# Performance work log

Measured on AMD Instinct MI355X. Metric: run time of the kernel, lower is better.

Reference implementation:

```python
import jax, jax.numpy as jnp
import numpy as np

N = 8192      # nodes
D_IN = 128    # input features
D_H = 48      # GAT hidden (hardcoded in module)
D_OUT = 32    # control output dim
NEG_INF = -9e15  # matches torch code's -9000000000000000.0


def setup_inputs() -> dict:
    key = jax.random.key(0)
    ks = jax.random.split(key, 12)
    s = 0.05
    return {
        "x": jax.random.normal(ks[0], (N, D_IN), jnp.float32),
        "adj": jax.random.randint(ks[1], (N, N), 0, 2, jnp.int32),
        "W_gat": jax.random.normal(ks[2], (D_H, D_IN), jnp.float32) * s,
        "a": jax.random.normal(ks[3], (1, D_H), jnp.float32) * s,
        "gamma": jnp.ones((D_H,), jnp.float32),
        "beta": jnp.zeros((D_H,), jnp.float32),
        "W1": jax.random.normal(ks[4], (256, D_H), jnp.float32) * s,
        "b1": jnp.zeros((256,), jnp.float32),
        "W2": jax.random.normal(ks[5], (128, 256), jnp.float32) * s,
        "b2": jnp.zeros((128,), jnp.float32),
        "W3": jax.random.normal(ks[6], (D_OUT, 128), jnp.float32) * s,
        "b3": jnp.zeros((D_OUT,), jnp.float32),
    }


def reference(x, adj, W_gat, a, gamma, beta, W1, b1, W2, b2, W3, b3):
    # --- LightweightGATLayer ---
    Wh = x @ W_gat.T                      # [N, D_H]
    s = Wh @ a.T                          # [N, 1] additive attention scores
    e = s + s.T                           # [N, N]
    e = jnp.where(e > 0, e, 0.2 * e)      # LeakyReLU(0.2)
    e = jnp.where(adj > 0, e, NEG_INF)    # mask non-edges
    attn = jax.nn.softmax(e, axis=1)      # row softmax; dropout is identity in eval
    h_prime = attn @ Wh                   # [N, D_H]
    # LayerNorm over last dim, eps=1e-5
    mu = jnp.mean(h_prime, axis=-1, keepdims=True)
    var = jnp.var(h_prime, axis=-1, keepdims=True)
    h = (h_prime - mu) * jax.lax.rsqrt(var + 1e-5) * gamma + beta
    # --- BiACT MLP head: 48 -> 256 -> 128 -> D_OUT ---
    h = jax.nn.relu(h @ W1.T + b1)
    h = jax.nn.relu(h @ W2.T + b2)
    return h @ W3.T + b3                  # [N, D_OUT]
```

## Files before the change

kernel.cpp:

```cpp
#include <hip/hip_runtime.h>

#define N 8192
#define DIN 128
#define DH 48
#define MT 128
#define KC 64
#define NSPLIT 16
#define JSPAN (N / NSPLIT)
#define NCHUNK (JSPAN / KC)
#define ACC_STRIDE 64
#define HSTR 49
#define RB 32

typedef _Float16 half8 __attribute__((ext_vector_type(8)));
typedef float f32x4 __attribute__((ext_vector_type(4)));

__global__ __launch_bounds__(256) void k_wh(const float* __restrict__ x,
                                            const float* __restrict__ Wg,
                                            float* __restrict__ Wh) {
    __shared__ float wT[DIN * DH];
    int t = threadIdx.x;
    for (int e = t; e < DIN * DH; e += 256) {
        int c = e / DIN, k = e % DIN;
        wT[k * DH + c] = Wg[e];
    }
    __syncthreads();
    int o = blockIdx.x * 256 + t;
    int r = o / DH, c = o % DH;
    const float4* xr = (const float4*)(x + (size_t)r * DIN);
    float acc = 0.f;
    #pragma unroll 8
    for (int k4 = 0; k4 < DIN / 4; ++k4) {
        float4 xv = xr[k4];
        int kb = k4 * 4;
        acc += xv.x * wT[(kb + 0) * DH + c];
        acc += xv.y * wT[(kb + 1) * DH + c];
        acc += xv.z * wT[(kb + 2) * DH + c];
        acc += xv.w * wT[(kb + 3) * DH + c];
    }
    Wh[o] = acc;
}

__global__ __launch_bounds__(256) void k_s(const float* __restrict__ Wh,
                                           const float* __restrict__ a,
                                           float* __restrict__ s) {
    int r = blockIdx.x * 256 + threadIdx.x;
    const float4* wr = (const float4*)(Wh + (size_t)r * DH);
    const float4* av = (const float4*)a;
    float acc = 0.f;
    #pragma unroll
    for (int k4 = 0; k4 < DH / 4; ++k4) {
        float4 w = wr[k4]; float4 aa = av[k4];
        acc += w.x * aa.x + w.y * aa.y + w.z * aa.z + w.w * aa.w;
    }
    s[r] = acc;
}

__global__ __launch_bounds__(256) void k_tr(const float* __restrict__ Wh,
                                            _Float16* __restrict__ WhT) {
    __shared__ _Float16 tile[DH][72];
    int t = threadIdx.x;
    int r0 = blockIdx.x * 64;
    for (int e = t; e < 64 * DH; e += 256) {
        int r = e / DH, c = e % DH;
        tile[c][r] = (_Float16)Wh[(size_t)(r0 + r) * DH + c];
    }
    __syncthreads();
    for (int u = t; u < DH * 8; u += 256) {
        int c = u >> 3, g = u & 7;
        *(half8*)&WhT[(size_t)c * N + r0 + g * 8] = *(const half8*)&tile[c][g * 8];
    }
}

__device__ inline half8 mk_p(float si, float4 sa, float4 sb, int4 m0, int4 m1) {
    float e0 = si + sa.x, e1 = si + sa.y, e2 = si + sa.z, e3 = si + sa.w;
    float e4 = si + sb.x, e5 = si + sb.y, e6 = si + sb.z, e7 = si + sb.w;
    e0 = fmaxf(e0, 0.2f * e0); e1 = fmaxf(e1, 0.2f * e1);
    e2 = fmaxf(e2, 0.2f * e2); e3 = fmaxf(e3, 0.2f * e3);
    e4 = fmaxf(e4, 0.2f * e4); e5 = fmaxf(e5, 0.2f * e5);
    e6 = fmaxf(e6, 0.2f * e6); e7 = fmaxf(e7, 0.2f * e7);
    half8 r;
    r[0] = (_Float16)(m0.x ? __expf(e0) : 0.f);
    r[1] = (_Float16)(m0.y ? __expf(e1) : 0.f);
    r[2] = (_Float16)(m0.z ? __expf(e2) : 0.f);
    r[3] = (_Float16)(m0.w ? __expf(e3) : 0.f);
    r[4] = (_Float16)(m1.x ? __expf(e4) : 0.f);
    r[5] = (_Float16)(m1.y ? __expf(e5) : 0.f);
    r[6] = (_Float16)(m1.z ? __expf(e6) : 0.f);
    r[7] = (_Float16)(m1.w ? __expf(e7) : 0.f);
    return r;
}

__global__ __launch_bounds__(256, 4) void k_gat(const int* __restrict__ adj,
                                                const _Float16* __restrict__ WhT,
                                                const float* __restrict__ s,
                                                float* __restrict__ accWs) {
    int t = threadIdx.x;
    int tile = blockIdx.x & 63;
    int split = blockIdx.x >> 6;
    int i0 = tile * MT;
    int jbase = split * JSPAN;

    int lane = t & 63, w = t >> 6;
    int ln16 = lane & 15, kq = lane >> 4;

    half8 bc;
    {
        _Float16 v = (ln16 == 0) ? (_Float16)1.0f : (_Float16)0.0f;
        #pragma unroll
        for (int i = 0; i < 8; ++i) bc[i] = v;
    }

    f32x4 acc[2][4];
    #pragma unroll
    for (int m = 0; m < 2; ++m)
        #pragma unroll
        for (int n = 0; n < 4; ++n) acc[m][n] = (f32x4){0.f, 0.f, 0.f, 0.f};

    const int row0 = i0 + w * 32 + ln16;
    const int row1 = row0 + 16;
    const float si0 = s[row0];
    const float si1 = s[row1];
    const int* ar0 = adj + (size_t)row0 * N;
    const int* ar1 = adj + (size_t)row1 * N;

    for (int chunk = 0; chunk < NCHUNK; ++chunk) {
        const int j0 = jbase + chunk * KC;
        const int jk0 = j0 + kq * 8;
        const int jk1 = jk0 + 32;

        int4 m00a = *(const int4*)(ar0 + jk0);
        int4 m00b = *(const int4*)(ar0 + jk0 + 4);
        int4 m01a = *(const int4*)(ar0 + jk1);
        int4 m01b = *(const int4*)(ar0 + jk1 + 4);
        int4 m10a = *(const int4*)(ar1 + jk0);
        int4 m10b = *(const int4*)(ar1 + jk0 + 4);
        int4 m11a = *(const int4*)(ar1 + jk1);
        int4 m11b = *(const int4*)(ar1 + jk1 + 4);
        float4 s0a = *(const float4*)(s + jk0);
        float4 s0b = *(const float4*)(s + jk0 + 4);
        float4 s1a = *(const float4*)(s + jk1);
        float4 s1b = *(const float4*)(s + jk1 + 4);
        half8 bf00 = *(const half8*)&WhT[(size_t)(0  + ln16) * N + jk0];
        half8 bf01 = *(const half8*)&WhT[(size_t)(16 + ln16) * N + jk0];
        half8 bf02 = *(const half8*)&WhT[(size_t)(32 + ln16) * N + jk0];
        half8 bf10 = *(const half8*)&WhT[(size_t)(0  + ln16) * N + jk1];
        half8 bf11 = *(const half8*)&WhT[(size_t)(16 + ln16) * N + jk1];
        half8 bf12 = *(const half8*)&WhT[(size_t)(32 + ln16) * N + jk1];

        half8 a00 = mk_p(si0, s0a, s0b, m00a, m00b);
        half8 a01 = mk_p(si0, s1a, s1b, m01a, m01b);
        half8 a10 = mk_p(si1, s0a, s0b, m10a, m10b);
        half8 a11 = mk_p(si1, s1a, s1b, m11a, m11b);

        acc[0][0] = __builtin_amdgcn_mfma_f32_16x16x32_f16(a00, bf00, acc[0][0], 0, 0, 0);
        acc[0][1] = __builtin_amdgcn_mfma_f32_16x16x32_f16(a00, bf01, acc[0][1], 0, 0, 0);
        acc[0][2] = __builtin_amdgcn_mfma_f32_16x16x32_f16(a00, bf02, acc[0][2], 0, 0, 0);
        acc[0][3] = __builtin_amdgcn_mfma_f32_16x16x32_f16(a00, bc,   acc[0][3], 0, 0, 0);
        acc[1][0] = __builtin_amdgcn_mfma_f32_16x16x32_f16(a10, bf00, acc[1][0], 0, 0, 0);
        acc[1][1] = __builtin_amdgcn_mfma_f32_16x16x32_f16(a10, bf01, acc[1][1], 0, 0, 0);
        acc[1][2] = __builtin_amdgcn_mfma_f32_16x16x32_f16(a10, bf02, acc[1][2], 0, 0, 0);
        acc[1][3] = __builtin_amdgcn_mfma_f32_16x16x32_f16(a10, bc,   acc[1][3], 0, 0, 0);
        acc[0][0] = __builtin_amdgcn_mfma_f32_16x16x32_f16(a01, bf10, acc[0][0], 0, 0, 0);
        acc[0][1] = __builtin_amdgcn_mfma_f32_16x16x32_f16(a01, bf11, acc[0][1], 0, 0, 0);
        acc[0][2] = __builtin_amdgcn_mfma_f32_16x16x32_f16(a01, bf12, acc[0][2], 0, 0, 0);
        acc[0][3] = __builtin_amdgcn_mfma_f32_16x16x32_f16(a01, bc,   acc[0][3], 0, 0, 0);
        acc[1][0] = __builtin_amdgcn_mfma_f32_16x16x32_f16(a11, bf10, acc[1][0], 0, 0, 0);
        acc[1][1] = __builtin_amdgcn_mfma_f32_16x16x32_f16(a11, bf11, acc[1][1], 0, 0, 0);
        acc[1][2] = __builtin_amdgcn_mfma_f32_16x16x32_f16(a11, bf12, acc[1][2], 0, 0, 0);
        acc[1][3] = __builtin_amdgcn_mfma_f32_16x16x32_f16(a11, bc,   acc[1][3], 0, 0, 0);
    }

    #pragma unroll
    for (int mtl = 0; mtl < 2; ++mtl) {
        size_t rbase = (size_t)split * N + i0 + w * 32 + mtl * 16 + kq * 4;
        #pragma unroll
        for (int nt = 0; nt < 4; ++nt) {
            int col = nt * 16 + ln16;
            if (nt == 3 && ln16 != 0) continue;
            #pragma unroll
            for (int reg = 0; reg < 4; ++reg)
                accWs[(rbase + reg) * ACC_STRIDE + col] = acc[mtl][nt][reg];
        }
    }
}

__global__ __launch_bounds__(256) void k_mlp(const float* __restrict__ accWs,
                                             const float* __restrict__ gamma,
                                             const float* __restrict__ beta,
                                             const float* __restrict__ W1, const float* __restrict__ b1,
                                             const float* __restrict__ W2, const float* __restrict__ b2,
                                             const float* __restrict__ W3, const float* __restrict__ b3,
                                             float* __restrict__ out) {
    __shared__ float hs[RB * HSTR];
    __shared__ float hN[RB * DH];
    __shared__ float h1[RB * 256];
    __shared__ float h2[RB * 128];
    int t = threadIdx.x;
    int r0 = blockIdx.x * RB;

    for (int e = t; e < RB * HSTR; e += 256) {
        int r = e / HSTR, d = e % HSTR;
        size_t base = (size_t)(r0 + r) * ACC_STRIDE + d;
        float v = 0.f;
        #pragma unroll
        for (int sp = 0; sp < NSPLIT; ++sp)
            v += accWs[(size_t)sp * N * ACC_STRIDE + base];
        hs[e] = v;
    }
    __syncthreads();

    if (t < RB) {
        float invl = 1.f / hs[t * HSTR + 48];
        float sum = 0.f;
        for (int d = 0; d < DH; ++d) sum += hs[t * HSTR + d];
        float mean = sum * invl * (1.f / DH);
        float var = 0.f;
        for (int d = 0; d < DH; ++d) {
            float dv = hs[t * HSTR + d] * invl - mean;
            var += dv * dv;
        }
        var *= (1.f / DH);
        float rs = rsqrtf(var + 1e-5f);
        for (int d = 0; d < DH; ++d) {
            float hv = (hs[t * HSTR + d] * invl - mean) * rs;
            hN[t * DH + d] = hv * gamma[d] + beta[d];
        }
    }
    __syncthreads();

    {
        int c0 = (t & 127) * 2, c1 = c0 + 1;
        int rbeg = (t >> 7) * 16;
        float4 wa[12], wb[12];
        const float4* wr0 = (const float4*)(W1 + c0 * DH);
        const float4* wr1 = (const float4*)(W1 + c1 * DH);
        #pragma unroll
        for (int k4 = 0; k4 < 12; ++k4) { wa[k4] = wr0[k4]; wb[k4] = wr1[k4]; }
        float ba = b1[c0], bb = b1[c1];
        for (int r = rbeg; r < rbeg + 16; ++r) {
            const float4* hv4 = (const float4*)&hN[r * DH];
            float a0 = ba, a1 = bb;
            #pragma unroll
            for (int k4 = 0; k4 < 12; ++k4) {
                float4 hv = hv4[k4];
                a0 += hv.x * wa[k4].x + hv.y * wa[k4].y + hv.z * wa[k4].z + hv.w * wa[k4].w;
                a1 += hv.x * wb[k4].x + hv.y * wb[k4].y + hv.z * wb[k4].z + hv.w * wb[k4].w;
            }
            h1[r * 256 + c0] = fmaxf(a0, 0.f);
            h1[r * 256 + c1] = fmaxf(a1, 0.f);
        }
    }
    __syncthreads();

    {
        int c4 = (t & 31) * 4;
        int rr0 = (t >> 5) * 4;
        float a[4][4];
        #pragma unroll
        for (int rr = 0; rr < 4; ++rr)
            #pragma unroll
            for (int cc = 0; cc < 4; ++cc) a[rr][cc] = 0.f;
        for (int k4 = 0; k4 < 64; ++k4) {
            float4 h[4], wv[4];
            #pragma unroll
            for (int rr = 0; rr < 4; ++rr)
                h[rr] = *(const float4*)&h1[(rr0 + rr) * 256 + 4 * k4];
            #pragma unroll
            for (int cc = 0; cc < 4; ++cc)
                wv[cc] = *(const float4*)&W2[(size_t)(c4 + cc) * 256 + 4 * k4];
            #pragma unroll
            for (int rr = 0; rr < 4; ++rr)
                #pragma unroll
                for (int cc = 0; cc < 4; ++cc)
                    a[rr][cc] += h[rr].x * wv[cc].x + h[rr].y * wv[cc].y
                               + h[rr].z * wv[cc].z + h[rr].w * wv[cc].w;
        }
        #pragma unroll
        for (int rr = 0; rr < 4; ++rr)
            #pragma unroll
            for (int cc = 0; cc < 4; ++cc)
                h2[(rr0 + rr) * 128 + c4 + cc] = fmaxf(a[rr][cc] + b2[c4 + cc], 0.f);
    }
    __syncthreads();

    {
        int c = t & 31;
        int rr0 = (t >> 5) * 4;
        float a[4];
        float bias = b3[c];
        #pragma unroll
        for (int rr = 0; rr < 4; ++rr) a[rr] = bias;
        const float4* wrow = (const float4*)(W3 + c * 128);
        for (int k4 = 0; k4 < 32; ++k4) {
            float4 wv = wrow[k4];
            #pragma unroll
            for (int rr = 0; rr < 4; ++rr) {
                float4 hv = *(const float4*)&h2[(rr0 + rr) * 128 + 4 * k4];
                a[rr] += wv.x * hv.x + wv.y * hv.y + wv.z * hv.z + wv.w * hv.w;
            }
        }
        #pragma unroll
        for (int rr = 0; rr < 4; ++rr)
            out[(size_t)(r0 + rr0 + rr) * 32 + c] = a[rr];
    }
}

extern "C" void kernel_launch(void* const* d_in, const int* in_sizes, int n_in,
                              void* d_out, int out_size, void* d_ws, size_t ws_size,
                              hipStream_t stream) {
    const float* x     = (const float*)d_in[0];
    const int*   adj   = (const int*)d_in[1];
    const float* Wg    = (const float*)d_in[2];
    const float* a     = (const float*)d_in[3];
    const float* gamma = (const float*)d_in[4];
    const float* beta  = (const float*)d_in[5];
    const float* W1    = (const float*)d_in[6];
    const float* b1    = (const float*)d_in[7];
    const float* W2    = (const float*)d_in[8];
    const float* b2    = (const float*)d_in[9];
    const float* W3    = (const float*)d_in[10];
    const float* b3    = (const float*)d_in[11];
    float* out = (float*)d_out;

    float* ws = (float*)d_ws;
    float*     Wh    = ws;
    float*     s     = ws + (size_t)N * DH;
    _Float16*  WhT   = (_Float16*)(ws + (size_t)N * DH + N);
    float*     accWs = ws + (size_t)N * DH + N + (size_t)N * DH / 2;

    k_wh<<<N * DH / 256, 256, 0, stream>>>(x, Wg, Wh);
    k_s<<<N / 256, 256, 0, stream>>>(Wh, a, s);
    k_tr<<<N / 64, 256, 0, stream>>>(Wh, WhT);
    k_gat<<<64 * NSPLIT, 256, 0, stream>>>(adj, WhT, s, accWs);
    k_mlp<<<N / RB, 256, 0, stream>>>(accWs, gamma, beta, W1, b1, W2, b2, W3, b3, out);
}
```

Baseline: 480.6 us.

## Pack adjacency into bitmask in a pre-pass and halve GAT j-splits

A new kernel streams the int32 adjacency matrix once with coalesced loads and uses wave ballots to compress it into a 64-bit-per-word bitmask. The attention kernel then reads the mask words instead of strided int4 loads from adj, which removes most of the memory traffic inside that kernel. The number of j-splits also drops from 16 to 8, which halves the partial-accumulator work but also halves the grid size and so the parallelism. The cost is an extra kernel launch plus an 8 MB mask buffer in the workspace.

Measured after the change: 518.1 us. 1.08x slower.

```diff
diff --git a/kernel.cpp b/kernel.cpp
--- a/kernel.cpp
+++ b/kernel.cpp
@@ -5,15 +5,31 @@
 #define DH 48
 #define MT 128
 #define KC 64
-#define NSPLIT 16
+#define NSPLIT 8
 #define JSPAN (N / NSPLIT)
 #define NCHUNK (JSPAN / KC)
+#define NW64 (N / 64)
 #define ACC_STRIDE 64
 #define HSTR 49
 #define RB 32
 
 typedef _Float16 half8 __attribute__((ext_vector_type(8)));
 typedef float f32x4 __attribute__((ext_vector_type(4)));
+
+__global__ __launch_bounds__(256) void k_pack(const int* __restrict__ adj,
+                                              unsigned long long* __restrict__ mask) {
+    int t = threadIdx.x;
+    int lane = t & 63, w = t >> 6;
+    size_t wid = (size_t)blockIdx.x * 4 + w;
+    size_t base = wid * 64;
+    const int* src = adj + base * 64 + lane;
+    #pragma unroll 4
+    for (int k = 0; k < 64; ++k) {
+        int v = src[(size_t)k * 64];
+        unsigned long long b = __ballot(v != 0);
+        if (lane == 0) mask[base + k] = b;
+    }
+}
 
 __global__ __launch_bounds__(256) void k_wh(const float* __restrict__ x,
                                             const float* __restrict__ Wg,
@@ -72,7 +88,7 @@
     }
 }
 
-__device__ inline half8 mk_p(float si, float4 sa, float4 sb, int4 m0, int4 m1) {
+__device__ inline half8 mk_p(float si, float4 sa, float4 sb, unsigned mb) {
     float e0 = si + sa.x, e1 = si + sa.y, e2 = si + sa.z, e3 = si + sa.w;
     float e4 = si + sb.x, e5 = si + sb.y, e6 = si + sb.z, e7 = si + sb.w;
     e0 = fmaxf(e0, 0.2f * e0); e1 = fmaxf(e1, 0.2f * e1);
@@ -80,18 +96,18 @@
     e4 = fmaxf(e4, 0.2f * e4); e5 = fmaxf(e5, 0.2f * e5);
     e6 = fmaxf(e6, 0.2f * e6); e7 = fmaxf(e7, 0.2f * e7);
     half8 r;
-    r[0] = (_Float16)(m0.x ? __expf(e0) : 0.f);
-    r[1] = (_Float16)(m0.y ? __expf(e1) : 0.f);
-    r[2] = (_Float16)(m0.z ? __expf(e2) : 0.f);
-    r[3] = (_Float16)(m0.w ? __expf(e3) : 0.f);
-    r[4] = (_Float16)(m1.x ? __expf(e4) : 0.f);
-    r[5] = (_Float16)(m1.y ? __expf(e5) : 0.f);
-    r[6] = (_Float16)(m1.z ? __expf(e6) : 0.f);
-    r[7] = (_Float16)(m1.w ? __expf(e7) : 0.f);
+    r[0] = (_Float16)((mb & 1u)   ? __expf(e0) : 0.f);
+    r[1] = (_Float16)((mb & 2u)   ? __expf(e1) : 0.f);
+    r[2] = (_Float16)((mb & 4u)   ? __expf(e2) : 0.f);
+    r[3] = (_Float16)((mb & 8u)   ? __expf(e3) : 0.f);
+    r[4] = (_Float16)((mb & 16u)  ? __expf(e4) : 0.f);
+    r[5] = (_Float16)((mb & 32u)  ? __expf(e5) : 0.f);
+    r[6] = (_Float16)((mb & 64u)  ? __expf(e6) : 0.f);
+    r[7] = (_Float16)((mb & 128u) ? __expf(e7) : 0.f);
     return r;
 }
 
-__global__ __launch_bounds__(256, 4) void k_gat(const int* __restrict__ adj,
+__global__ __launch_bounds__(256, 4) void k_gat(const unsigned long long* __restrict__ mask,
                                                 const _Float16* __restrict__ WhT,
                                                 const float* __restrict__ s,
                                                 float* __restrict__ accWs) {
@@ -121,22 +137,16 @@
     const int row1 = row0 + 16;
     const float si0 = s[row0];
     const float si1 = s[row1];
-    const int* ar0 = adj + (size_t)row0 * N;
-    const int* ar1 = adj + (size_t)row1 * N;
+    const unsigned long long* mr0 = mask + (size_t)row0 * NW64 + (jbase >> 6);
+    const unsigned long long* mr1 = mask + (size_t)row1 * NW64 + (jbase >> 6);
 
     for (int chunk = 0; chunk < NCHUNK; ++chunk) {
         const int j0 = jbase + chunk * KC;
         const int jk0 = j0 + kq * 8;
         const int jk1 = jk0 + 32;
 
-        int4 m00a = *(const int4*)(ar0 + jk0);
-        int4 m00b = *(const int4*)(ar0 + jk0 + 4);
-        int4 m01a = *(const int4*)(ar0 + jk1);
-        int4 m01b = *(const int4*)(ar0 + jk1 + 4);
-        int4 m10a = *(const int4*)(ar1 + jk0);
-        int4 m10b = *(const int4*)(ar1 + jk0 + 4);
-        int4 m11a = *(const int4*)(ar1 + jk1);
-        int4 m11b = *(const int4*)(ar1 + jk1 + 4);
+        unsigned long long mw0 = mr0[chunk];
+        unsigned long long mw1 = mr1[chunk];
         float4 s0a = *(const float4*)(s + jk0);
         float4 s0b = *(const float4*)(s + jk0 + 4);
         float4 s1a = *(const float4*)(s + jk1);
@@ -148,10 +158,15 @@
         half8 bf11 = *(const half8*)&WhT[(size_t)(16 + ln16) * N + jk1];
         half8 bf12 = *(const half8*)&WhT[(size_t)(32 + ln16) * N + jk1];
 
-        half8 a00 = mk_p(si0, s0a, s0b, m00a, m00b);
-        half8 a01 = mk_p(si0, s1a, s1b, m01a, m01b);
-        half8 a10 = mk_p(si1, s0a, s0b, m10a, m10b);
-        half8 a11 = mk_p(si1, s1a, s1b, m11a, m11b);
+        unsigned b00 = (unsigned)(mw0 >> (kq * 8)) & 0xffu;
+        unsigned b01 = (unsigned)(mw0 >> (kq * 8 + 32)) & 0xffu;
+        unsigned b10 = (unsigned)(mw1 >> (kq * 8)) & 0xffu;
+        unsigned b11 = (unsigned)(mw1 >> (kq * 8 + 32)) & 0xffu;
+
+        half8 a00 = mk_p(si0, s0a, s0b, b00);
+        half8 a01 = mk_p(si0, s1a, s1b, b01);
+        half8 a10 = mk_p(si1, s0a, s0b, b10);
+        half8 a11 = mk_p(si1, s1a, s1b, b11);
 
         acc[0][0] = __builtin_amdgcn_mfma_f32_16x16x32_f16(a00, bf00, acc[0][0], 0, 0, 0);
         acc[0][1] = __builtin_amdgcn_mfma_f32_16x16x32_f16(a00, bf01, acc[0][1], 0, 0, 0);
@@ -324,14 +339,16 @@
     float* out = (float*)d_out;
 
     float* ws = (float*)d_ws;
-    float*     Wh    = ws;
-    float*     s     = ws + (size_t)N * DH;
-    _Float16*  WhT   = (_Float16*)(ws + (size_t)N * DH + N);
-    float*     accWs = ws + (size_t)N * DH + N + (size_t)N * DH / 2;
-
+    float*              Wh    = ws;
+    float*              s     = Wh + (size_t)N * DH;
+    _Float16*           WhT   = (_Float16*)(s + N);
+    unsigned long long* mask  = (unsigned long long*)(WhT + (size_t)N * DH);
+    float*              accWs = (float*)(mask + (size_t)N * NW64);
+
+    k_pack<<<N * N / 64 / 256, 256, 0, stream>>>(adj, mask);
     k_wh<<<N * DH / 256, 256, 0, stream>>>(x, Wg, Wh);
     k_s<<<N / 256, 256, 0, stream>>>(Wh, a, s);
     k_tr<<<N / 64, 256, 0, stream>>>(Wh, WhT);
-    k_gat<<<64 * NSPLIT, 256, 0, stream>>>(adj, WhT, s, accWs);
+    k_gat<<<64 * NSPLIT, 256, 0, stream>>>(mask, WhT, s, accWs);
     k_mlp<<<N / RB, 256, 0, stream>>>(accWs, gamma, beta, W1, b1, W2, b2, W3, b3, out);
 }
```
